# Optimization experiments

Measured on AMD Instinct MI355X. Metric: run time of the kernel, lower is better.

The kernel has to match this reference:

```python
import jax, jax.numpy as jnp
import numpy as np

DEPTH, HEADS, DIM, DHEAD, MLP = 4, 16, 1024, 64, 4096
B, N, M = 4, 1024, 1024
EPS = 1e-5


def layer_norm(x, w, b):
    mu = jnp.mean(x, axis=-1, keepdims=True)
    var = jnp.var(x, axis=-1, keepdims=True)
    return (x - mu) * jax.lax.rsqrt(var + EPS) * w + b


def setup_inputs() -> dict:
    key = jax.random.key(0)
    ks = jax.random.split(key, 16)
    inner = HEADS * DHEAD
    s = lambda fan_in: 1.0 / np.sqrt(fan_in)
    # weights stored in (in, out) layout: y = x @ W + b
    return {
        "x": jax.random.normal(ks[0], (B, N, DIM), jnp.float32),
        "m": jax.random.normal(ks[1], (B, M, DIM), jnp.float32),
        "Wq": jax.random.normal(ks[2], (DEPTH, DIM, inner), jnp.float32) * s(DIM),
        "Wk": jax.random.normal(ks[3], (DEPTH, DIM, inner), jnp.float32) * s(DIM),
        "Wv": jax.random.normal(ks[4], (DEPTH, DIM, inner), jnp.float32) * s(DIM),
        "Wo": jax.random.normal(ks[5], (DEPTH, inner, DIM), jnp.float32) * s(inner),
        "bo": jnp.zeros((DEPTH, DIM), jnp.float32),
        "ln1_w": jnp.ones((DEPTH, DIM), jnp.float32),
        "ln1_b": jnp.zeros((DEPTH, DIM), jnp.float32),
        "W1": jax.random.normal(ks[6], (DEPTH, DIM, MLP), jnp.float32) * s(DIM),
        "b1": jnp.zeros((DEPTH, MLP), jnp.float32),
        "W2": jax.random.normal(ks[7], (DEPTH, MLP, DIM), jnp.float32) * s(MLP),
        "b2": jnp.zeros((DEPTH, DIM), jnp.float32),
        "ln2_w": jnp.ones((DEPTH, DIM), jnp.float32),
        "ln2_b": jnp.zeros((DEPTH, DIM), jnp.float32),
    }


def reference(x, m, Wq, Wk, Wv, Wo, bo, ln1_w, ln1_b, W1, b1, W2, b2, ln2_w, ln2_b):
    scale = DIM ** (-0.5)  # NOTE: original scales by dim**-0.5, not dim_head**-0.5
    for i in range(DEPTH):
        # cross-attention block (PreNorm on x only; m is used raw, as in source)
        h = layer_norm(x, ln1_w[i], ln1_b[i])
        q = jnp.einsum('bnd,de->bne', h, Wq[i]).reshape(B, N, HEADS, DHEAD)
        k = jnp.einsum('bmd,de->bme', m, Wk[i]).reshape(B, M, HEADS, DHEAD)
        v = jnp.einsum('bmd,de->bme', m, Wv[i]).reshape(B, M, HEADS, DHEAD)
        dots = jnp.einsum('bihd,bjhd->bhij', q, k) * scale
        attn = jax.nn.softmax(dots, axis=-1)
        out = jnp.einsum('bhij,bjhd->bihd', attn, v).reshape(B, N, HEADS * DHEAD)
        x = x + jnp.einsum('bne,ed->bnd', out, Wo[i]) + bo[i]
        # feed-forward block
        h2 = layer_norm(x, ln2_w[i], ln2_b[i])
        ff = jax.nn.gelu(jnp.einsum('bnd,df->bnf', h2, W1[i]) + b1[i], approximate=False)
        x = x + jnp.einsum('bnf,fd->bnd', ff, W2[i]) + b2[i]
    return x
```

## Files before the change

kernel.cpp:

```cpp
#include <hip/hip_runtime.h>
#include <hip/hip_bf16.h>
#include <math.h>

typedef __hip_bfloat16 bf16;
typedef __attribute__((ext_vector_type(8))) short bf16x8;
typedef __attribute__((ext_vector_type(4))) float f32x4;

#define DEPTH  4
#define HEADS  16
#define DIM    1024
#define DHEAD  64
#define MLPD   4096
#define BB     4
#define NN     1024
#define MMK    1024
#define ROWS   (BB*NN)
#define QKVS   3072

__device__ inline float bitsbf(short s) {
  union { float f; unsigned u; } c; c.u = ((unsigned)(unsigned short)s) << 16; return c.f;
}
__device__ inline short bfbits(float f) {
  bf16 h = __float2bfloat16(f); return *(short*)&h;
}

__device__ inline void gload_lds16(const bf16* g, bf16* l) {
  __builtin_amdgcn_global_load_lds((const __attribute__((address_space(1))) unsigned int*)g,
                                   (__attribute__((address_space(3))) unsigned int*)l, 16, 0, 0);
}

__global__ __launch_bounds__(256) void f2b_kernel(const float* __restrict__ in, bf16* __restrict__ out, int n) {
  int i = blockIdx.x * 256 + threadIdx.x;
  if (i < n) out[i] = __float2bfloat16(in[i]);
}

__global__ __launch_bounds__(256) void transpose_f2b(const float* __restrict__ in, bf16* __restrict__ out,
                                                     int inStride, int rowOff, int colOff, int outStride) {
  __shared__ float tile[32][33];
  int n0 = blockIdx.x * 32, k0 = blockIdx.y * 32;
  int tx = threadIdx.x, ty = threadIdx.y;
  #pragma unroll
  for (int i = 0; i < 32; i += 8)
    tile[ty + i][tx] = in[(size_t)(rowOff + k0 + ty + i) * inStride + colOff + n0 + tx];
  __syncthreads();
  #pragma unroll
  for (int i = 0; i < 32; i += 8)
    out[(size_t)(n0 + ty + i) * outStride + k0 + tx] = __float2bfloat16(tile[tx][ty + i]);
}

__global__ __launch_bounds__(256) void ln_kernel(const float* __restrict__ x, const float* __restrict__ w,
                                                 const float* __restrict__ b, bf16* __restrict__ out) {
  int row = blockIdx.x, t = threadIdx.x;
  const float* xr = x + (size_t)row * DIM;
  float4 xv = *(const float4*)(xr + t * 4);
  float s  = xv.x + xv.y + xv.z + xv.w;
  float s2 = xv.x * xv.x + xv.y * xv.y + xv.z * xv.z + xv.w * xv.w;
  #pragma unroll
  for (int off = 32; off; off >>= 1) { s += __shfl_xor(s, off, 64); s2 += __shfl_xor(s2, off, 64); }
  __shared__ float sh_s[4], sh_s2[4], sh_mu, sh_rstd;
  int wid = t >> 6;
  if ((t & 63) == 0) { sh_s[wid] = s; sh_s2[wid] = s2; }
  __syncthreads();
  if (t == 0) {
    float S1 = sh_s[0] + sh_s[1] + sh_s[2] + sh_s[3];
    float S2 = sh_s2[0] + sh_s2[1] + sh_s2[2] + sh_s2[3];
    float mu = S1 * (1.0f / DIM);
    float var = S2 * (1.0f / DIM) - mu * mu;
    sh_mu = mu; sh_rstd = rsqrtf(var + 1e-5f);
  }
  __syncthreads();
  float mu = sh_mu, rstd = sh_rstd;
  float4 wv = *(const float4*)(w + t * 4);
  float4 bv = *(const float4*)(b + t * 4);
  bf16* orow = out + (size_t)row * DIM + t * 4;
  orow[0] = __float2bfloat16((xv.x - mu) * rstd * wv.x + bv.x);
  orow[1] = __float2bfloat16((xv.y - mu) * rstd * wv.y + bv.y);
  orow[2] = __float2bfloat16((xv.z - mu) * rstd * wv.z + bv.z);
  orow[3] = __float2bfloat16((xv.w - mu) * rstd * wv.w + bv.w);
}

#define MODE_PLAIN 0
#define MODE_GELU  1
#define MODE_RES   2
#define BM 128
#define BK 32

template<int JT>
__global__ __launch_bounds__(256) void gemm_tile(const bf16* __restrict__ A, const bf16* __restrict__ Bt,
                                                 const float* __restrict__ bias, bf16* __restrict__ outb,
                                                 float* __restrict__ resf, int outStride, int K, int mode) {
  constexpr int BN = JT * 32;
  __shared__ __align__(16) bf16 As[BM * BK];
  __shared__ __align__(16) bf16 Bs[BN * BK];
  int t = threadIdx.x;
  int w = t >> 6, l = t & 63;
  int l15 = l & 15, quad = l >> 4;
  int col0 = blockIdx.x * BN, row0 = blockIdx.y * BM;
  int wm = (w >> 1) * 64, wn = (w & 1) * (JT * 16);

  f32x4 acc[4][JT] = {};

  int sm = w * 16 + (l >> 2);
  int sk = (l & 3) * 8;
  const bf16* ag0 = A  + (size_t)(row0 + sm) * K + sk;
  const bf16* ag1 = A  + (size_t)(row0 + 64 + sm) * K + sk;
  const bf16* bg0 = Bt + (size_t)(col0 + sm) * K + sk;
  const bf16* bg1 = Bt + (size_t)(col0 + 64 + sm) * K + sk;
  bf16* lA0 = As + w * 512;
  bf16* lA1 = As + 2048 + w * 512;
  bf16* lB0 = Bs + w * 512;
  bf16* lB1 = Bs + 2048 + w * 512;

  for (int k0 = 0; k0 < K; k0 += BK) {
    gload_lds16(ag0 + k0, lA0);
    gload_lds16(ag1 + k0, lA1);
    gload_lds16(bg0 + k0, lB0);
    if constexpr (JT == 4) gload_lds16(bg1 + k0, lB1);
    __syncthreads();
    bf16x8 af[4], bfr[JT];
    #pragma unroll
    for (int i = 0; i < 4; ++i)  af[i]  = *(const bf16x8*)&As[(wm + i * 16 + l15) * BK + quad * 8];
    #pragma unroll
    for (int j = 0; j < JT; ++j) bfr[j] = *(const bf16x8*)&Bs[(wn + j * 16 + l15) * BK + quad * 8];
    #pragma unroll
    for (int i = 0; i < 4; ++i)
      #pragma unroll
      for (int j = 0; j < JT; ++j)
        acc[i][j] = __builtin_amdgcn_mfma_f32_16x16x32_bf16(af[i], bfr[j], acc[i][j], 0, 0, 0);
    __syncthreads();
  }

  #pragma unroll
  for (int i = 0; i < 4; ++i) {
    #pragma unroll
    for (int j = 0; j < JT; ++j) {
      int gcol = col0 + wn + j * 16 + l15;
      float bval = (mode != MODE_PLAIN && bias != nullptr) ? bias[gcol] : 0.0f;
      #pragma unroll
      for (int r = 0; r < 4; ++r) {
        int grow = row0 + wm + i * 16 + quad * 4 + r;
        float val = acc[i][j][r];
        size_t idx = (size_t)grow * outStride + gcol;
        if (mode == MODE_RES) {
          resf[idx] = resf[idx] + val + bval;
        } else {
          if (mode == MODE_GELU) {
            float u = val + bval;
            val = 0.5f * u * (1.0f + erff(u * 0.70710678118654752f));
          }
          outb[idx] = __float2bfloat16(val);
        }
      }
    }
  }
}

#define ALDP 72

__global__ __launch_bounds__(256) void attn_mfma_kernel(const bf16* __restrict__ qkv, bf16* __restrict__ o) {
  __shared__ __align__(16) short Kl[64][ALDP];
  __shared__ __align__(16) short Vt[64][ALDP];
  __shared__ __align__(16) short Pl[64][ALDP];

  int t = threadIdx.x;
  int lane = t & 63, w = t >> 6;
  int l15 = lane & 15, quad = lane >> 4;
  int qt = blockIdx.x;
  int bh = blockIdx.y;
  int b = bh >> 4, hh = bh & 15;

  const bf16* q = qkv;
  const bf16* k = qkv + 1024;
  const bf16* v = qkv + 2048;

  bf16x8 qfrag[2];
  {
    const bf16* qp = q + (size_t)(b * NN + qt * 64 + w * 16 + l15) * QKVS + hh * DHEAD + quad * 8;
    #pragma unroll
    for (int ks = 0; ks < 2; ++ks) {
      bf16x8 raw = *(const bf16x8*)(qp + ks * 32);
      bf16x8 sc;
      #pragma unroll
      for (int e = 0; e < 8; ++e) sc[e] = bfbits(bitsbf(raw[e]) * 0.03125f);
      qfrag[ks] = sc;
    }
  }

  f32x4 Oacc[4] = {{}, {}, {}, {}};
  float mrow[4] = {-1e30f, -1e30f, -1e30f, -1e30f};
  float lrow[4] = {0.f, 0.f, 0.f, 0.f};

  int srow = t >> 2, sc0 = (t & 3) * 16;

  for (int kt = 0; kt < MMK / 64; ++kt) {
    __syncthreads();
    {
      const bf16* kp = k + (size_t)(b * MMK + kt * 64 + srow) * QKVS + hh * DHEAD + sc0;
      *(bf16x8*)&Kl[srow][sc0]     = *(const bf16x8*)kp;
      *(bf16x8*)&Kl[srow][sc0 + 8] = *(const bf16x8*)(kp + 8);
      const bf16* vp = v + (size_t)(b * MMK + kt * 64 + srow) * QKVS + hh * DHEAD + sc0;
      bf16x8 v0 = *(const bf16x8*)vp;
      bf16x8 v1 = *(const bf16x8*)(vp + 8);
      #pragma unroll
      for (int e = 0; e < 8; ++e) {
        Vt[sc0 + e][srow]     = v0[e];
        Vt[sc0 + 8 + e][srow] = v1[e];
      }
    }
    __syncthreads();

    f32x4 S[4] = {{}, {}, {}, {}};
    #pragma unroll
    for (int ks = 0; ks < 2; ++ks) {
      #pragma unroll
      for (int j = 0; j < 4; ++j) {
        bf16x8 bfr = *(const bf16x8*)&Kl[j * 16 + l15][ks * 32 + quad * 8];
        S[j] = __builtin_amdgcn_mfma_f32_16x16x32_bf16(qfrag[ks], bfr, S[j], 0, 0, 0);
      }
    }

    #pragma unroll
    for (int r = 0; r < 4; ++r) {
      float tm = fmaxf(fmaxf(S[0][r], S[1][r]), fmaxf(S[2][r], S[3][r]));
      tm = fmaxf(tm, __shfl_xor(tm, 1, 64));
      tm = fmaxf(tm, __shfl_xor(tm, 2, 64));
      tm = fmaxf(tm, __shfl_xor(tm, 4, 64));
      tm = fmaxf(tm, __shfl_xor(tm, 8, 64));
      float mn = fmaxf(mrow[r], tm);
      float alpha = __expf(mrow[r] - mn);
      mrow[r] = mn;
      float rs = 0.f;
      #pragma unroll
      for (int j = 0; j < 4; ++j) {
        float p = __expf(S[j][r] - mn);
        S[j][r] = p;
        rs += p;
      }
      rs += __shfl_xor(rs, 1, 64);
      rs += __shfl_xor(rs, 2, 64);
      rs += __shfl_xor(rs, 4, 64);
      rs += __shfl_xor(rs, 8, 64);
      lrow[r] = lrow[r] * alpha + rs;
      #pragma unroll
      for (int j = 0; j < 4; ++j) {
        Oacc[j][r] *= alpha;
        Pl[w * 16 + quad * 4 + r][j * 16 + l15] = bfbits(S[j][r]);
      }
    }
    __syncthreads();

    #pragma unroll
    for (int ks = 0; ks < 2; ++ks) {
      bf16x8 pa = *(const bf16x8*)&Pl[w * 16 + l15][ks * 32 + quad * 8];
      #pragma unroll
      for (int j = 0; j < 4; ++j) {
        bf16x8 vb = *(const bf16x8*)&Vt[j * 16 + l15][ks * 32 + quad * 8];
        Oacc[j] = __builtin_amdgcn_mfma_f32_16x16x32_bf16(pa, vb, Oacc[j], 0, 0, 0);
      }
    }
  }

  #pragma unroll
  for (int r = 0; r < 4; ++r) {
    float inv = 1.0f / lrow[r];
    bf16* op = o + (size_t)(b * NN + qt * 64 + w * 16 + quad * 4 + r) * DIM + hh * DHEAD;
    #pragma unroll
    for (int j = 0; j < 4; ++j)
      op[j * 16 + l15] = __float2bfloat16(Oacc[j][r] * inv);
  }
}

extern "C" void kernel_launch(void* const* d_in, const int* in_sizes, int n_in,
                              void* d_out, int out_size, void* d_ws, size_t ws_size,
                              hipStream_t stream) {
  const float* x_in = (const float*)d_in[0];
  const float* m    = (const float*)d_in[1];
  const float* Wq   = (const float*)d_in[2];
  const float* Wk   = (const float*)d_in[3];
  const float* Wv   = (const float*)d_in[4];
  const float* Wo   = (const float*)d_in[5];
  const float* bo   = (const float*)d_in[6];
  const float* ln1w = (const float*)d_in[7];
  const float* ln1b = (const float*)d_in[8];
  const float* W1   = (const float*)d_in[9];
  const float* b1   = (const float*)d_in[10];
  const float* W2   = (const float*)d_in[11];
  const float* b2   = (const float*)d_in[12];
  const float* ln2w = (const float*)d_in[13];
  const float* ln2b = (const float*)d_in[14];

  float* xf = (float*)d_out;

  char* ws = (char*)d_ws;
  bf16* h    = (bf16*)(ws + 0);
  bf16* mb   = (bf16*)(ws + (8u  << 20));
  bf16* qkv  = (bf16*)(ws + (16u << 20));
  bf16* ffh  = (bf16*)(ws + (16u << 20));
  bf16* wt   = (bf16*)(ws + (40u << 20));

  const int NTOK = ROWS * DIM;

  hipMemcpyAsync(xf, x_in, (size_t)NTOK * sizeof(float), hipMemcpyDeviceToDevice, stream);
  f2b_kernel<<<dim3((NTOK + 255) / 256), dim3(256), 0, stream>>>(m, mb, NTOK);

  dim3 blk(256);
  dim3 tblk(32, 8);
  dim3 g_n1(DIM / 64, ROWS / BM);
  dim3 g_n2(2048 / 128, ROWS / BM);
  dim3 tr_1k(DIM / 32, DIM / 32);
  dim3 tr_w1(2048 / 32, DIM / 32);
  dim3 tr_w2(DIM / 32, 2048 / 32);
  dim3 attn_grid(NN / 64, BB * HEADS);

  for (int L = 0; L < DEPTH; ++L) {
    const float* WqL = Wq + (size_t)L * DIM * DIM;
    const float* WkL = Wk + (size_t)L * DIM * DIM;
    const float* WvL = Wv + (size_t)L * DIM * DIM;
    const float* WoL = Wo + (size_t)L * DIM * DIM;
    const float* W1L = W1 + (size_t)L * DIM * MLPD;
    const float* W2L = W2 + (size_t)L * MLPD * DIM;

    ln_kernel<<<dim3(ROWS), blk, 0, stream>>>(xf, ln1w + L * DIM, ln1b + L * DIM, h);

    transpose_f2b<<<tr_1k, tblk, 0, stream>>>(WkL, wt, DIM, 0, 0, DIM);
    transpose_f2b<<<tr_1k, tblk, 0, stream>>>(WvL, wt + 1024 * 1024, DIM, 0, 0, DIM);
    gemm_tile<4><<<g_n2, blk, 0, stream>>>(mb, wt, nullptr, qkv + 1024, nullptr, QKVS, DIM, MODE_PLAIN);

    transpose_f2b<<<tr_1k, tblk, 0, stream>>>(WqL, wt, DIM, 0, 0, DIM);
    gemm_tile<2><<<g_n1, blk, 0, stream>>>(h, wt, nullptr, qkv, nullptr, QKVS, DIM, MODE_PLAIN);

    attn_mfma_kernel<<<attn_grid, blk, 0, stream>>>(qkv, h);

    transpose_f2b<<<tr_1k, tblk, 0, stream>>>(WoL, wt, DIM, 0, 0, DIM);
    gemm_tile<2><<<g_n1, blk, 0, stream>>>(h, wt, bo + L * DIM, nullptr, xf, DIM, DIM, MODE_RES);

    ln_kernel<<<dim3(ROWS), blk, 0, stream>>>(xf, ln2w + L * DIM, ln2b + L * DIM, h);

    for (int half = 0; half < 2; ++half) {
      transpose_f2b<<<tr_w1, tblk, 0, stream>>>(W1L, wt, MLPD, 0, half * 2048, DIM);
      gemm_tile<4><<<g_n2, blk, 0, stream>>>(h, wt, b1 + (size_t)L * MLPD + half * 2048, ffh, nullptr,
                                             2048, DIM, MODE_GELU);
      transpose_f2b<<<tr_w2, tblk, 0, stream>>>(W2L, wt, DIM, half * 2048, 0, 2048);
      gemm_tile<2><<<g_n1, blk, 0, stream>>>(ffh, wt, (half == 0) ? (b2 + (size_t)L * DIM) : nullptr,
                                             nullptr, xf, DIM, 2048, MODE_RES);
    }
  }
}
```

Baseline: 1.786 ms.

## Double-buffer GEMM LDS tiles and swap attention grid axes

Measured after the change: 1.695 ms. 5.1% less time.

```diff
diff --git a/kernel.cpp b/kernel.cpp
--- a/kernel.cpp
+++ b/kernel.cpp
@@ -90,8 +90,8 @@
                                                  const float* __restrict__ bias, bf16* __restrict__ outb,
                                                  float* __restrict__ resf, int outStride, int K, int mode) {
   constexpr int BN = JT * 32;
-  __shared__ __align__(16) bf16 As[BM * BK];
-  __shared__ __align__(16) bf16 Bs[BN * BK];
+  __shared__ __align__(16) bf16 As[2][BM * BK];
+  __shared__ __align__(16) bf16 Bs[2][BN * BK];
   int t = threadIdx.x;
   int w = t >> 6, l = t & 63;
   int l15 = l & 15, quad = l >> 4;
@@ -106,28 +106,33 @@
   const bf16* ag1 = A  + (size_t)(row0 + 64 + sm) * K + sk;
   const bf16* bg0 = Bt + (size_t)(col0 + sm) * K + sk;
   const bf16* bg1 = Bt + (size_t)(col0 + 64 + sm) * K + sk;
-  bf16* lA0 = As + w * 512;
-  bf16* lA1 = As + 2048 + w * 512;
-  bf16* lB0 = Bs + w * 512;
-  bf16* lB1 = Bs + 2048 + w * 512;
-
+
+  gload_lds16(ag0, &As[0][w * 512]);
+  gload_lds16(ag1, &As[0][2048 + w * 512]);
+  gload_lds16(bg0, &Bs[0][w * 512]);
+  if constexpr (JT == 4) gload_lds16(bg1, &Bs[0][2048 + w * 512]);
+
+  int cur = 0;
   for (int k0 = 0; k0 < K; k0 += BK) {
-    gload_lds16(ag0 + k0, lA0);
-    gload_lds16(ag1 + k0, lA1);
-    gload_lds16(bg0 + k0, lB0);
-    if constexpr (JT == 4) gload_lds16(bg1 + k0, lB1);
     __syncthreads();
+    int nxt = cur ^ 1;
+    if (k0 + BK < K) {
+      gload_lds16(ag0 + k0 + BK, &As[nxt][w * 512]);
+      gload_lds16(ag1 + k0 + BK, &As[nxt][2048 + w * 512]);
+      gload_lds16(bg0 + k0 + BK, &Bs[nxt][w * 512]);
+      if constexpr (JT == 4) gload_lds16(bg1 + k0 + BK, &Bs[nxt][2048 + w * 512]);
+    }
     bf16x8 af[4], bfr[JT];
     #pragma unroll
-    for (int i = 0; i < 4; ++i)  af[i]  = *(const bf16x8*)&As[(wm + i * 16 + l15) * BK + quad * 8];
-    #pragma unroll
-    for (int j = 0; j < JT; ++j) bfr[j] = *(const bf16x8*)&Bs[(wn + j * 16 + l15) * BK + quad * 8];
+    for (int i = 0; i < 4; ++i)  af[i]  = *(const bf16x8*)&As[cur][(wm + i * 16 + l15) * BK + quad * 8];
+    #pragma unroll
+    for (int j = 0; j < JT; ++j) bfr[j] = *(const bf16x8*)&Bs[cur][(wn + j * 16 + l15) * BK + quad * 8];
     #pragma unroll
     for (int i = 0; i < 4; ++i)
       #pragma unroll
       for (int j = 0; j < JT; ++j)
         acc[i][j] = __builtin_amdgcn_mfma_f32_16x16x32_bf16(af[i], bfr[j], acc[i][j], 0, 0, 0);
-    __syncthreads();
+    cur = nxt;
   }
 
   #pragma unroll
@@ -165,8 +170,8 @@
   int t = threadIdx.x;
   int lane = t & 63, w = t >> 6;
   int l15 = lane & 15, quad = lane >> 4;
-  int qt = blockIdx.x;
-  int bh = blockIdx.y;
+  int bh = blockIdx.x;
+  int qt = blockIdx.y;
   int b = bh >> 4, hh = bh & 15;
 
   const bf16* q = qkv;
@@ -310,7 +315,7 @@
   dim3 tr_1k(DIM / 32, DIM / 32);
   dim3 tr_w1(2048 / 32, DIM / 32);
   dim3 tr_w2(DIM / 32, 2048 / 32);
-  dim3 attn_grid(NN / 64, BB * HEADS);
+  dim3 attn_grid(BB * HEADS, NN / 64);
 
   for (int L = 0; L < DEPTH; ++L) {
     const float* WqL = Wq + (size_t)L * DIM * DIM;
```
